# Performance work log

Measured on AMD Instinct MI355X. Metric: run time of the kernel, lower is better.

Reference implementation:

```python
import jax, jax.numpy as jnp
import numpy as np

B, N, M, D, H = 4, 384, 384, 64, 64


def _lin(key, fi, fo):
    kw, kb = jax.random.split(key)
    bound = 1.0 / np.sqrt(fi)
    W = jax.random.uniform(kw, (fi, fo), jnp.float32, -bound, bound)
    b = jax.random.uniform(kb, (fo,), jnp.float32, -bound, bound)
    return W, b


def setup_inputs() -> dict:
    key = jax.random.key(0)
    kX, kY, kp = jax.random.split(key, 3)
    X = jax.random.normal(kX, (B, N, D), jnp.float32)
    Y = jax.random.normal(kY, (B, M, D), jnp.float32)
    ks = jax.random.split(kp, 10)
    inp = {"X": X, "Y": Y}
    # Four pair encoders (e1_xx, e1_xy, e1_yx, e1_yy): Linear(2D,H) -> ReLU -> Linear(H,H)
    for i, tag in enumerate(["xx", "xy", "yx", "yy"]):
        W1, b1 = _lin(ks[2 * i], 2 * D, H)
        W2, b2 = _lin(ks[2 * i + 1], H, H)
        inp[f"W_{tag}1"], inp[f"b_{tag}1"] = W1, b1
        inp[f"W_{tag}2"], inp[f"b_{tag}2"] = W2, b2
    # Decoder: Linear(2H,H) -> ReLU -> Linear(H,1)
    inp["Wd1"], inp["bd1"] = _lin(ks[8], 2 * H, H)
    inp["Wd2"], inp["bd2"] = _lin(ks[9], H, 1)
    return inp


def _pair_branch(A, C, W1, b1, W2, b2):
    """Encode pairs cat(A[b,j], C[b,i]) with MLP, then max over j.

    Instead of materializing the [B,I,J,2D] concat tensor, split the first
    linear layer: cat(a, c) @ W1 == a @ W1[:D] + c @ W1[D:].
    Returns [B, I, H].
    """
    Da = A.shape[-1]
    pa = jnp.einsum('bjd,dh->bjh', A, W1[:Da])   # contribution of A[b, j]
    pc = jnp.einsum('bid,dh->bih', C, W1[Da:])   # contribution of C[b, i]
    pre = pa[:, None, :, :] + pc[:, :, None, :] + b1          # [B, I, J, H]
    h = jnp.einsum('bijh,hk->bijk', jax.nn.relu(pre), W2) + b2  # [B, I, J, H]
    return jnp.max(h, axis=2)                                   # [B, I, H]


def reference(X, Y,
              W_xx1, b_xx1, W_xx2, b_xx2,
              W_xy1, b_xy1, W_xy2, b_xy2,
              W_yx1, b_yx1, W_yx2, b_yx2,
              W_yy1, b_yy1, W_yy2, b_yy2,
              Wd1, bd1, Wd2, bd2):
    # XX[b,i,j] = cat(X[b,j], X[b,i]); YX[b,i,j] = cat(Y[b,j], X[b,i]); etc.
    Z_XX = _pair_branch(X, X, W_xx1, b_xx1, W_xx2, b_xx2)  # [B, N, H]
    Z_YX = _pair_branch(Y, X, W_yx1, b_yx1, W_yx2, b_yx2)  # [B, N, H]
    # Computed in the original forward but never used downstream (dead code):
    Z_YY = _pair_branch(Y, Y, W_yy1, b_yy1, W_yy2, b_yy2)  # noqa: F841
    Z_XY = _pair_branch(X, Y, W_xy1, b_xy1, W_xy2, b_xy2)  # noqa: F841
    # Original source sets Z_Y = Z_XX - Z_YX as well (apparent bug, preserved).
    diff = Z_XX - Z_YX
    Z_X = jnp.sum(diff, axis=1)  # [B, H]
    Z_Y = jnp.sum(diff, axis=1)  # [B, H]
    z = jnp.concatenate([Z_X, Z_Y], axis=-1)        # [B, 2H]
    h = jax.nn.relu(z @ Wd1 + bd1)
    return h @ Wd2 + bd2                             # [B, 1]
```

## Files before the change

### kernel.cpp

```cpp
#include <hip/hip_runtime.h>

#define B_ 4
#define N_ 384
#define D_ 64
#define H_ 64
#define BN_ (B_ * N_)
#define ROW_ (N_ * H_)
#define NTP_ 12
#define LDW_ 68

typedef float f32x4 __attribute__((ext_vector_type(4)));
typedef _Float16 half8 __attribute__((ext_vector_type(8)));
typedef __fp16 fp16x2 __attribute__((ext_vector_type(2)));

union frag_cast { f32x4 f; half8 h; };

__global__ __launch_bounds__(256) void proj_kernel(
    const float* __restrict__ X, const float* __restrict__ Y,
    const float* __restrict__ Wxx1, const float* __restrict__ bxx1,
    const float* __restrict__ Wyx1, const float* __restrict__ byx1,
    const float* __restrict__ W2xx, const float* __restrict__ W2yx,
    float* __restrict__ PAxx, float* __restrict__ PCxx,
    float* __restrict__ PAyx, float* __restrict__ PCyx,
    _Float16* __restrict__ W2F)
{
    if (blockIdx.x >= BN_) {
        int t = (blockIdx.x - BN_) * 256 + threadIdx.x;
        int br = t >> 10;
        int q  = (t >> 6) & 15;
        int l  = t & 63;
        int nt = q >> 2, kt = (q >> 1) & 1, part = q & 1;
        const float* W2 = br ? W2yx : W2xx;
        int n = nt * 16 + (l & 15);
        int g = l >> 4;
        _Float16* dst = W2F + t * 8;
#pragma unroll
        for (int e = 0; e < 8; ++e) {
            int h = kt * 32 + g * 8 + e;
            float v = W2[h * 64 + n];
            _Float16 hi = (_Float16)v;
            _Float16 lo = (_Float16)(v - (float)hi);
            dst[e] = part ? lo : hi;
        }
        return;
    }

    int blk = blockIdx.x;
    int t = threadIdx.x;
    int which = t >> 6, h = t & 63;

    __shared__ float xrow[64];
    __shared__ float yrow[64];
    if (t < 64) xrow[t] = X[blk * 64 + t];
    else if (t < 128) yrow[t - 64] = Y[blk * 64 + (t - 64)];
    __syncthreads();

    const float* v = (which == 2) ? yrow : xrow;
    const float* W = (which < 2) ? Wxx1 : Wyx1;
    int rowoff = (which & 1) ? 64 : 0;

    float acc = 0.f;
    if (which == 1) acc = bxx1[h];
    if (which == 3) acc = byx1[h];
#pragma unroll
    for (int d = 0; d < 64; ++d)
        acc = fmaf(v[d], W[(rowoff + d) * 64 + h], acc);

    float* dst = (which == 0) ? PAxx : (which == 1) ? PCxx
               : (which == 2) ? PAyx : PCyx;
    dst[blk * 64 + h] = acc;
}

__global__ __launch_bounds__(256, 3) void pair_mfma_kernel(
    const float* __restrict__ PAxx, const float* __restrict__ PCxx,
    const float* __restrict__ PAyx, const float* __restrict__ PCyx,
    const f32x4* __restrict__ W2F,
    float* __restrict__ zxxs, float* __restrict__ zyxs)
{
    int bid = blockIdx.x;
    int blk = (bid & 7) * 96 + (bid >> 3);
    int br = blk / 384;
    int ig = blk % 384;
    int t = threadIdx.x;
    int w = t >> 6, l = t & 63;
    int g = l >> 4, m = l & 15;
    int bi = ig * 4 + w;
    int b  = bi / N_;

    const float* PA = br ? PAyx : PAxx;
    const float* PC = br ? PCyx : PCxx;

    __shared__ float lbuf[2][32 * LDW_];
    __shared__ float zsums[4][64];

    half8 bf[4][2][2];
    const f32x4* Wb = W2F + br * 1024;
#pragma unroll
    for (int q = 0; q < 16; ++q) {
        frag_cast u;
        u.f = Wb[q * 64 + l];
        asm volatile("" : "+v"(u.f));
        bf[q >> 2][(q >> 1) & 1][q & 1] = u.h;
    }

    f32x4 pcq[4];
#pragma unroll
    for (int kt = 0; kt < 2; ++kt) {
        pcq[kt * 2 + 0] = *(const f32x4*)(PC + bi * 64 + kt * 32 + g * 8);
        pcq[kt * 2 + 1] = *(const f32x4*)(PC + bi * 64 + kt * 32 + g * 8 + 4);
    }

    float mm[4] = {-3.0e38f, -3.0e38f, -3.0e38f, -3.0e38f};

    int srow = t >> 4;
    int scg  = t & 15;
    const float* gsrc = PA + b * ROW_ + srow * 64 + scg * 4;
    int soff = srow * LDW_ + scg * 4;

    *(f32x4*)(&lbuf[0][0] + soff) = *(const f32x4*)(gsrc);
    *(f32x4*)(&lbuf[0][0] + soff + 16 * LDW_) = *(const f32x4*)(gsrc + 1024);
    __syncthreads();

    const f32x4 vzero = {0.f, 0.f, 0.f, 0.f};
    int cur = 0;

#pragma unroll 1
    for (int pt = 0; pt < NTP_; ++pt) {
        f32x4 gn0, gn1;
        if (pt + 1 < NTP_) {
            gn0 = *(const f32x4*)(gsrc + (pt + 1) * 2048);
            gn1 = *(const f32x4*)(gsrc + (pt + 1) * 2048 + 1024);
        }

#pragma unroll
        for (int st = 0; st < 2; ++st) {
            const float* lrd = &lbuf[0][0] + cur * (32 * LDW_)
                             + (st * 16 + m) * LDW_ + g * 8;
            f32x4 s0 = *(const f32x4*)(lrd);
            f32x4 s1 = *(const f32x4*)(lrd + 4);
            f32x4 s2 = *(const f32x4*)(lrd + 32);
            f32x4 s3 = *(const f32x4*)(lrd + 36);

            half8 ah[2], al[2];
#pragma unroll
            for (int kt = 0; kt < 2; ++kt) {
                f32x4 xa = (kt ? s2 : s0) + pcq[kt * 2 + 0];
                f32x4 xb = (kt ? s3 : s1) + pcq[kt * 2 + 1];
                xa = __builtin_elementwise_max(xa, vzero);
                xb = __builtin_elementwise_max(xb, vzero);
                fp16x2* ahp = (fp16x2*)&ah[kt];
                fp16x2* alp = (fp16x2*)&al[kt];
#pragma unroll
                for (int p2 = 0; p2 < 2; ++p2) {
                    fp16x2 hpa = __builtin_amdgcn_cvt_pkrtz(xa[p2 * 2], xa[p2 * 2 + 1]);
                    fp16x2 hpb = __builtin_amdgcn_cvt_pkrtz(xb[p2 * 2], xb[p2 * 2 + 1]);
                    ahp[p2]     = hpa;
                    ahp[p2 + 2] = hpb;
                    alp[p2]     = __builtin_amdgcn_cvt_pkrtz(xa[p2 * 2]     - (float)hpa[0],
                                                             xa[p2 * 2 + 1] - (float)hpa[1]);
                    alp[p2 + 2] = __builtin_amdgcn_cvt_pkrtz(xb[p2 * 2]     - (float)hpb[0],
                                                             xb[p2 * 2 + 1] - (float)hpb[1]);
                }
            }

#pragma unroll
            for (int nt = 0; nt < 4; ++nt) {
                f32x4 a = {0.f, 0.f, 0.f, 0.f};
#pragma unroll
                for (int kt = 0; kt < 2; ++kt) {
                    a = __builtin_amdgcn_mfma_f32_16x16x32_f16(ah[kt], bf[nt][kt][0], a, 0, 0, 0);
                    a = __builtin_amdgcn_mfma_f32_16x16x32_f16(ah[kt], bf[nt][kt][1], a, 0, 0, 0);
                    a = __builtin_amdgcn_mfma_f32_16x16x32_f16(al[kt], bf[nt][kt][0], a, 0, 0, 0);
                }
                mm[nt] = fmaxf(mm[nt],
                               fmaxf(fmaxf(a[0], a[1]), fmaxf(a[2], a[3])));
            }
        }

        if (pt + 1 < NTP_) {
            *(f32x4*)(&lbuf[0][0] + (cur ^ 1) * (32 * LDW_) + soff) = gn0;
            *(f32x4*)(&lbuf[0][0] + (cur ^ 1) * (32 * LDW_) + soff + 16 * LDW_) = gn1;
        }
        __syncthreads();
        cur ^= 1;
    }

#pragma unroll
    for (int nt = 0; nt < 4; ++nt) {
        float v = mm[nt];
        v = fmaxf(v, __shfl_xor(v, 16));
        v = fmaxf(v, __shfl_xor(v, 32));
        mm[nt] = v;
    }
    float z = (l < 32) ? ((l < 16) ? mm[0] : mm[1])
                       : ((l < 48) ? mm[2] : mm[3]);

    zsums[w][l] = z;
    __syncthreads();
    if (w == 0) {
        float s = ((zsums[0][l] + zsums[1][l]) + zsums[2][l]) + zsums[3][l];
        (br ? zyxs : zxxs)[ig * 64 + l] = s;
    }
}

__global__ __launch_bounds__(256) void head_kernel(
    const float* __restrict__ zxxs, const float* __restrict__ zyxs,
    const float* __restrict__ b2xx, const float* __restrict__ b2yx,
    const float* __restrict__ Wd1, const float* __restrict__ bd1,
    const float* __restrict__ Wd2, const float* __restrict__ bd2,
    float* __restrict__ out)
{
    int b = blockIdx.x;
    int t = threadIdx.x;
    int ig = t >> 6, h = t & 63;

    __shared__ float sbuf[4][64];
    __shared__ float zx[64];

    float s = 0.f;
    for (int q = ig; q < 96; q += 4) {
        int idx = (b * 96 + q) * 64 + h;
        s += zxxs[idx] - zyxs[idx];
    }
    sbuf[ig][h] = s;
    __syncthreads();
    if (t < 64)
        zx[t] = sbuf[0][t] + sbuf[1][t] + sbuf[2][t] + sbuf[3][t]
              + (float)N_ * (b2xx[t] - b2yx[t]);
    __syncthreads();

    if (t < 64) {
        float acc = bd1[t];
#pragma unroll
        for (int d = 0; d < 64; ++d)
            acc = fmaf(zx[d], Wd1[d * 64 + t] + Wd1[(64 + d) * 64 + t], acc);
        float h1 = fmaxf(acc, 0.f);
        float r = h1 * Wd2[t];
#pragma unroll
        for (int off = 32; off; off >>= 1) r += __shfl_down(r, off);
        if (t == 0) out[b] = r + bd2[0];
    }
}

extern "C" void kernel_launch(void* const* d_in, const int* in_sizes, int n_in,
                              void* d_out, int out_size, void* d_ws, size_t ws_size,
                              hipStream_t stream) {
    const float* X    = (const float*)d_in[0];
    const float* Y    = (const float*)d_in[1];
    const float* Wxx1 = (const float*)d_in[2];
    const float* bxx1 = (const float*)d_in[3];
    const float* W2xx = (const float*)d_in[4];
    const float* b2xx = (const float*)d_in[5];
    const float* Wyx1 = (const float*)d_in[10];
    const float* byx1 = (const float*)d_in[11];
    const float* W2yx = (const float*)d_in[12];
    const float* b2yx = (const float*)d_in[13];
    const float* Wd1  = (const float*)d_in[18];
    const float* bd1  = (const float*)d_in[19];
    const float* Wd2  = (const float*)d_in[20];
    const float* bd2  = (const float*)d_in[21];

    float* ws   = (float*)d_ws;
    float* PAxx = ws;
    float* PCxx = ws + 1 * (BN_ * H_);
    float* PAyx = ws + 2 * (BN_ * H_);
    float* PCyx = ws + 3 * (BN_ * H_);
    float* zxxs = ws + 4 * (BN_ * H_);
    float* zyxs = ws + 4 * (BN_ * H_) + 384 * 64;
    _Float16* W2F = (_Float16*)(ws + 5 * (BN_ * H_));

    proj_kernel<<<BN_ + 8, 256, 0, stream>>>(X, Y, Wxx1, bxx1, Wyx1, byx1,
                                             W2xx, W2yx,
                                             PAxx, PCxx, PAyx, PCyx, W2F);
    pair_mfma_kernel<<<768, 256, 0, stream>>>(PAxx, PCxx, PAyx, PCyx,
                                              (const f32x4*)W2F, zxxs, zyxs);
    head_kernel<<<B_, 256, 0, stream>>>(zxxs, zyxs, b2xx, b2yx,
                                        Wd1, bd1, Wd2, bd2, (float*)d_out);
}
```

Baseline: 47.92 us.

## Process two i-rows per wave in pair kernel and four rows per proj block

The pair kernel now runs 128-thread blocks where each wave handles two i-rows, so every LDS read of a PA tile feeds two sets of MFMA computations. The projection kernel computes four rows per block so each W1 load is reused four times, and its grid shrinks accordingly. The aim is to cut LDS and global traffic per unit of work. The cost is higher register pressure and fewer waves per block, which may lower latency hiding. The staging loop now loads 8 rows per pass with 4 passes to cover the 32-row tile.

```diff
diff --git a/kernel.cpp b/kernel.cpp
--- a/kernel.cpp
+++ b/kernel.cpp
@@ -24,8 +24,8 @@
     float* __restrict__ PAyx, float* __restrict__ PCyx,
     _Float16* __restrict__ W2F)
 {
-    if (blockIdx.x >= BN_) {
-        int t = (blockIdx.x - BN_) * 256 + threadIdx.x;
+    if (blockIdx.x >= 384) {
+        int t = (blockIdx.x - 384) * 256 + threadIdx.x;
         int br = t >> 10;
         int q  = (t >> 6) & 15;
         int l  = t & 63;
@@ -49,29 +49,39 @@
     int t = threadIdx.x;
     int which = t >> 6, h = t & 63;
 
-    __shared__ float xrow[64];
-    __shared__ float yrow[64];
-    if (t < 64) xrow[t] = X[blk * 64 + t];
-    else if (t < 128) yrow[t - 64] = Y[blk * 64 + (t - 64)];
-    __syncthreads();
-
-    const float* v = (which == 2) ? yrow : xrow;
+    __shared__ float xr[4][64];
+    __shared__ float yr[4][64];
+    xr[t >> 6][t & 63] = X[(blk * 4 + (t >> 6)) * 64 + (t & 63)];
+    yr[t >> 6][t & 63] = Y[(blk * 4 + (t >> 6)) * 64 + (t & 63)];
+    __syncthreads();
+
+    const float (*v)[64] = (which == 2) ? yr : xr;
     const float* W = (which < 2) ? Wxx1 : Wyx1;
     int rowoff = (which & 1) ? 64 : 0;
 
-    float acc = 0.f;
-    if (which == 1) acc = bxx1[h];
-    if (which == 3) acc = byx1[h];
-#pragma unroll
-    for (int d = 0; d < 64; ++d)
-        acc = fmaf(v[d], W[(rowoff + d) * 64 + h], acc);
+    float acc[4];
+    float binit = 0.f;
+    if (which == 1) binit = bxx1[h];
+    if (which == 3) binit = byx1[h];
+#pragma unroll
+    for (int r = 0; r < 4; ++r) acc[r] = binit;
+
+#pragma unroll
+    for (int d = 0; d < 64; ++d) {
+        float wv = W[(rowoff + d) * 64 + h];
+#pragma unroll
+        for (int r = 0; r < 4; ++r)
+            acc[r] = fmaf(v[r][d], wv, acc[r]);
+    }
 
     float* dst = (which == 0) ? PAxx : (which == 1) ? PCxx
                : (which == 2) ? PAyx : PCyx;
-    dst[blk * 64 + h] = acc;
+#pragma unroll
+    for (int r = 0; r < 4; ++r)
+        dst[(blk * 4 + r) * 64 + h] = acc[r];
 }
 
-__global__ __launch_bounds__(256, 3) void pair_mfma_kernel(
+__global__ __launch_bounds__(128, 3) void pair_mfma_kernel(
     const float* __restrict__ PAxx, const float* __restrict__ PCxx,
     const float* __restrict__ PAyx, const float* __restrict__ PCyx,
     const f32x4* __restrict__ W2F,
@@ -84,8 +94,8 @@
     int t = threadIdx.x;
     int w = t >> 6, l = t & 63;
     int g = l >> 4, m = l & 15;
-    int bi = ig * 4 + w;
-    int b  = bi / N_;
+    int bi0 = ig * 4 + w * 2;
+    int b  = (ig * 4) / N_;
 
     const float* PA = br ? PAyx : PAxx;
     const float* PC = br ? PCyx : PCxx;
@@ -103,22 +113,26 @@
         bf[q >> 2][(q >> 1) & 1][q & 1] = u.h;
     }
 
-    f32x4 pcq[4];
+    f32x4 pcq0[4], pcq1[4];
 #pragma unroll
     for (int kt = 0; kt < 2; ++kt) {
-        pcq[kt * 2 + 0] = *(const f32x4*)(PC + bi * 64 + kt * 32 + g * 8);
-        pcq[kt * 2 + 1] = *(const f32x4*)(PC + bi * 64 + kt * 32 + g * 8 + 4);
-    }
-
-    float mm[4] = {-3.0e38f, -3.0e38f, -3.0e38f, -3.0e38f};
-
-    int srow = t >> 4;
-    int scg  = t & 15;
-    const float* gsrc = PA + b * ROW_ + srow * 64 + scg * 4;
-    int soff = srow * LDW_ + scg * 4;
-
-    *(f32x4*)(&lbuf[0][0] + soff) = *(const f32x4*)(gsrc);
-    *(f32x4*)(&lbuf[0][0] + soff + 16 * LDW_) = *(const f32x4*)(gsrc + 1024);
+        pcq0[kt * 2 + 0] = *(const f32x4*)(PC + bi0 * 64 + kt * 32 + g * 8);
+        pcq0[kt * 2 + 1] = *(const f32x4*)(PC + bi0 * 64 + kt * 32 + g * 8 + 4);
+        pcq1[kt * 2 + 0] = *(const f32x4*)(PC + (bi0 + 1) * 64 + kt * 32 + g * 8);
+        pcq1[kt * 2 + 1] = *(const f32x4*)(PC + (bi0 + 1) * 64 + kt * 32 + g * 8 + 4);
+    }
+
+    float mm0[4] = {-3.0e38f, -3.0e38f, -3.0e38f, -3.0e38f};
+    float mm1[4] = {-3.0e38f, -3.0e38f, -3.0e38f, -3.0e38f};
+
+    int sr = t >> 4;
+    int scg = t & 15;
+    const float* gsrc = PA + b * ROW_ + sr * 64 + scg * 4;
+
+#pragma unroll
+    for (int r = 0; r < 4; ++r)
+        *(f32x4*)(&lbuf[0][0] + (sr + 8 * r) * LDW_ + scg * 4) =
+            *(const f32x4*)(gsrc + r * 512);
     __syncthreads();
 
     const f32x4 vzero = {0.f, 0.f, 0.f, 0.f};
@@ -126,10 +140,11 @@
 
 #pragma unroll 1
     for (int pt = 0; pt < NTP_; ++pt) {
-        f32x4 gn0, gn1;
+        f32x4 gn[4];
         if (pt + 1 < NTP_) {
-            gn0 = *(const f32x4*)(gsrc + (pt + 1) * 2048);
-            gn1 = *(const f32x4*)(gsrc + (pt + 1) * 2048 + 1024);
+#pragma unroll
+            for (int r = 0; r < 4; ++r)
+                gn[r] = *(const f32x4*)(gsrc + (pt + 1) * 2048 + r * 512);
         }
 
 #pragma unroll
@@ -141,61 +156,78 @@
             f32x4 s2 = *(const f32x4*)(lrd + 32);
             f32x4 s3 = *(const f32x4*)(lrd + 36);
 
-            half8 ah[2], al[2];
-#pragma unroll
-            for (int kt = 0; kt < 2; ++kt) {
-                f32x4 xa = (kt ? s2 : s0) + pcq[kt * 2 + 0];
-                f32x4 xb = (kt ? s3 : s1) + pcq[kt * 2 + 1];
-                xa = __builtin_elementwise_max(xa, vzero);
-                xb = __builtin_elementwise_max(xb, vzero);
-                fp16x2* ahp = (fp16x2*)&ah[kt];
-                fp16x2* alp = (fp16x2*)&al[kt];
-#pragma unroll
-                for (int p2 = 0; p2 < 2; ++p2) {
-                    fp16x2 hpa = __builtin_amdgcn_cvt_pkrtz(xa[p2 * 2], xa[p2 * 2 + 1]);
-                    fp16x2 hpb = __builtin_amdgcn_cvt_pkrtz(xb[p2 * 2], xb[p2 * 2 + 1]);
-                    ahp[p2]     = hpa;
-                    ahp[p2 + 2] = hpb;
-                    alp[p2]     = __builtin_amdgcn_cvt_pkrtz(xa[p2 * 2]     - (float)hpa[0],
-                                                             xa[p2 * 2 + 1] - (float)hpa[1]);
-                    alp[p2 + 2] = __builtin_amdgcn_cvt_pkrtz(xb[p2 * 2]     - (float)hpb[0],
-                                                             xb[p2 * 2 + 1] - (float)hpb[1]);
+#pragma unroll
+            for (int ii = 0; ii < 2; ++ii) {
+                const f32x4* pcq = ii ? pcq1 : pcq0;
+                float* mm = ii ? mm1 : mm0;
+
+                half8 ah[2], al[2];
+#pragma unroll
+                for (int kt = 0; kt < 2; ++kt) {
+                    f32x4 xa = (kt ? s2 : s0) + pcq[kt * 2 + 0];
+                    f32x4 xb = (kt ? s3 : s1) + pcq[kt * 2 + 1];
+                    xa = __builtin_elementwise_max(xa, vzero);
+                    xb = __builtin_elementwise_max(xb, vzero);
+                    fp16x2* ahp = (fp16x2*)&ah[kt];
+                    fp16x2* alp = (fp16x2*)&al[kt];
+#pragma unroll
+                    for (int p2 = 0; p2 < 2; ++p2) {
+                        fp16x2 hpa = __builtin_amdgcn_cvt_pkrtz(xa[p2 * 2], xa[p2 * 2 + 1]);
+                        fp16x2 hpb = __builtin_amdgcn_cvt_pkrtz(xb[p2 * 2], xb[p2 * 2 + 1]);
+                        ahp[p2]     = hpa;
+                        ahp[p2 + 2] = hpb;
+                        alp[p2]     = __builtin_amdgcn_cvt_pkrtz(xa[p2 * 2]     - (float)hpa[0],
+                                                                 xa[p2 * 2 + 1] - (float)hpa[1]);
+                        alp[p2 + 2] = __builtin_amdgcn_cvt_pkrtz(xb[p2 * 2]     - (float)hpb[0],
+                                                                 xb[p2 * 2 + 1] - (float)hpb[1]);
+                    }
                 }
+
+#pragma unroll
+                for (int nt = 0; nt < 4; ++nt) {
+                    f32x4 a = {0.f, 0.f, 0.f, 0.f};
+#pragma unroll
+                    for (int kt = 0; kt < 2; ++kt) {
+                        a = __builtin_amdgcn_mfma_f32_16x16x32_f16(ah[kt], bf[nt][kt][0], a, 0, 0, 0);
+                        a = __builtin_amdgcn_mfma_f32_16x16x32_f16(ah[kt], bf[nt][kt][1], a, 0, 0, 0);
+                        a = __builtin_amdgcn_mfma_f32_16x16x32_f16(al[kt], bf[nt][kt][0], a, 0, 0, 0);
+                    }
+                    mm[nt] = fmaxf(mm[nt],
+                                   fmaxf(fmaxf(a[0], a[1]), fmaxf(a[2], a[3])));
+                }
+                __builtin_amdgcn_sched_barrier(0);
             }
-
-#pragma unroll
-            for (int nt = 0; nt < 4; ++nt) {
-                f32x4 a = {0.f, 0.f, 0.f, 0.f};
-#pragma unroll
-                for (int kt = 0; kt < 2; ++kt) {
-                    a = __builtin_amdgcn_mfma_f32_16x16x32_f16(ah[kt], bf[nt][kt][0], a, 0, 0, 0);
-                    a = __builtin_amdgcn_mfma_f32_16x16x32_f16(ah[kt], bf[nt][kt][1], a, 0, 0, 0);
-                    a = __builtin_amdgcn_mfma_f32_16x16x32_f16(al[kt], bf[nt][kt][0], a, 0, 0, 0);
-                }
-                mm[nt] = fmaxf(mm[nt],
-                               fmaxf(fmaxf(a[0], a[1]), fmaxf(a[2], a[3])));
-            }
         }
 
         if (pt + 1 < NTP_) {
-            *(f32x4*)(&lbuf[0][0] + (cur ^ 1) * (32 * LDW_) + soff) = gn0;
-            *(f32x4*)(&lbuf[0][0] + (cur ^ 1) * (32 * LDW_) + soff + 16 * LDW_) = gn1;
+#pragma unroll
+            for (int r = 0; r < 4; ++r)
+                *(f32x4*)(&lbuf[0][0] + (cur ^ 1) * (32 * LDW_)
+                          + (sr + 8 * r) * LDW_ + scg * 4) = gn[r];
         }
         __syncthreads();
         cur ^= 1;
     }
 
-#pragma unroll
-    for (int nt = 0; nt < 4; ++nt) {
-        float v = mm[nt];
-        v = fmaxf(v, __shfl_xor(v, 16));
-        v = fmaxf(v, __shfl_xor(v, 32));
-        mm[nt] = v;
-    }
-    float z = (l < 32) ? ((l < 16) ? mm[0] : mm[1])
-                       : ((l < 48) ? mm[2] : mm[3]);
-
-    zsums[w][l] = z;
+    float z0, z1;
+    {
+        float v0[4], v1[4];
+#pragma unroll
+        for (int nt = 0; nt < 4; ++nt) {
+            float a = mm0[nt];
+            a = fmaxf(a, __shfl_xor(a, 16));
+            a = fmaxf(a, __shfl_xor(a, 32));
+            v0[nt] = a;
+            float c = mm1[nt];
+            c = fmaxf(c, __shfl_xor(c, 16));
+            c = fmaxf(c, __shfl_xor(c, 32));
+            v1[nt] = c;
+        }
+        z0 = (l < 32) ? ((l < 16) ? v0[0] : v0[1]) : ((l < 48) ? v0[2] : v0[3]);
+        z1 = (l < 32) ? ((l < 16) ? v1[0] : v1[1]) : ((l < 48) ? v1[2] : v1[3]);
+    }
+    zsums[w * 2 + 0][l] = z0;
+    zsums[w * 2 + 1][l] = z1;
     __syncthreads();
     if (w == 0) {
         float s = ((zsums[0][l] + zsums[1][l]) + zsums[2][l]) + zsums[3][l];
@@ -269,10 +301,10 @@
     float* zyxs = ws + 4 * (BN_ * H_) + 384 * 64;
     _Float16* W2F = (_Float16*)(ws + 5 * (BN_ * H_));
 
-    proj_kernel<<<BN_ + 8, 256, 0, stream>>>(X, Y, Wxx1, bxx1, Wyx1, byx1,
+    proj_kernel<<<384 + 8, 256, 0, stream>>>(X, Y, Wxx1, bxx1, Wyx1, byx1,
                                              W2xx, W2yx,
                                              PAxx, PCxx, PAyx, PCyx, W2F);
-    pair_mfma_kernel<<<768, 256, 0, stream>>>(PAxx, PCxx, PAyx, PCyx,
+    pair_mfma_kernel<<<768, 128, 0, stream>>>(PAxx, PCxx, PAyx, PCyx,
                                               (const f32x4*)W2F, zxxs, zyxs);
     head_kernel<<<B_, 256, 0, stream>>>(zxxs, zyxs, b2xx, b2yx,
                                         Wd1, bd1, Wd2, bd2, (float*)d_out);
```

New measurement: 79.37 us. +65.6%, slower.
